# Kernel tuning notes

Measured on AMD Instinct MI355X. Metric: run time of the kernel, lower is better.

Reference implementation:

```python
import jax, jax.numpy as jnp
import numpy as np

B, N, F_IN, F_OUT = 64, 1024, 200, 200
NEG_SLOPE = 0.2  # PyG GATConv default


def setup_inputs() -> dict:
    key = jax.random.key(0)
    k1, k2, k3, k4, k5 = jax.random.split(key, 5)
    return {
        "x": jax.random.normal(k1, (B, 1, N, F_IN), dtype=jnp.float32),
        "W": jax.random.normal(k2, (F_IN, F_OUT), dtype=jnp.float32) * 0.05,
        "att_src": jax.random.normal(k3, (F_OUT,), dtype=jnp.float32) * 0.05,
        "att_dst": jax.random.normal(k4, (F_OUT,), dtype=jnp.float32) * 0.05,
        "bias": jax.random.normal(k5, (F_OUT,), dtype=jnp.float32) * 0.05,
    }


def reference(x, W, att_src, att_dst, bias):
    # x: [B, 1, N, F_IN]; module flattens to (B*N) nodes but the edge_index
    # only spans node ids 0..N-1 (complete graph minus self loops). PyG's
    # GATConv re-adds self loops for ALL B*N nodes, so:
    #   nodes 0..N-1 : dense softmax attention over all N nodes (incl. self)
    #   nodes >= N   : only the self loop -> out = h_i + bias
    b, _, n, f = x.shape
    xf = x.reshape(b * n, f)
    h = xf @ W                                # [B*N, F_OUT] linear transform

    h0 = h[:n]                                # first graph's nodes
    a_s = h0 @ att_src                        # [N] per-source score
    a_d = h0 @ att_dst                        # [N] per-target score
    # score[i, j] = leaky_relu(a_dst[i] + a_src[j]), softmax over sources j
    scores = jax.nn.leaky_relu(a_d[:, None] + a_s[None, :], negative_slope=NEG_SLOPE)
    alpha = jax.nn.softmax(scores, axis=1)    # [N, N]
    out0 = alpha @ h0 + bias                  # [N, F_OUT]

    out_rest = h[n:] + bias                   # self-loop only -> alpha == 1
    out = jnp.concatenate([out0, out_rest], axis=0)
    return out.reshape(b, n, -1)[:, None]     # [B, 1, N, F_OUT]
```

## Files before the change

### kernel.cpp

```cpp
#include <hip/hip_runtime.h>

#define BATCH 64
#define NNODE 1024
#define FDIM  200
#define MROWS (BATCH * NNODE)
#define NEG_SLOPE 0.2f

#define NKT 7
#define NNT 13
#define KTBYTES (NNT * 1024)
#define KSPLIT 4

typedef short s16x8 __attribute__((ext_vector_type(8)));
typedef float f32x4 __attribute__((ext_vector_type(4)));


__device__ __forceinline__ unsigned int f2bf(float f) {
    unsigned int u = __float_as_uint(f);
    return (u + 0x7fffu + ((u >> 16) & 1u)) >> 16;
}
__device__ __forceinline__ unsigned int pack2(float a, float b) {
    return f2bf(a) | (f2bf(b) << 16);
}

__global__ __launch_bounds__(64) void k_prep(const float* __restrict__ W,
                                             const float* __restrict__ att_src,
                                             const float* __restrict__ att_dst,
                                             unsigned short* __restrict__ fragW,
                                             float* __restrict__ wsv,
                                             float* __restrict__ wdv)
{
    const int b    = blockIdx.x;
    const int lane = threadIdx.x;

    if (b < 91) {
        const int kt   = b / NNT;
        const int nt   = b - kt * NNT;
        const int n    = nt * 16 + (lane & 15);
        const int kb   = kt * 32 + (lane >> 4) * 8;
        s16x8 v;
        #pragma unroll
        for (int j = 0; j < 8; ++j) {
            int k = kb + j;
            float f = (k < FDIM && n < FDIM) ? W[k * FDIM + n] : 0.f;
            v[j] = (short)f2bf(f);
        }
        ((s16x8*)(fragW + (size_t)b * 512))[lane] = v;
    } else {
        const int kk = b - 91;
        const float* Wr = W + kk * FDIM;
        float ps = 0.f, pd = 0.f;
        #pragma unroll
        for (int i = 0; i < 4; ++i) {
            int n = lane + i * 64;
            if (n < FDIM) {
                float wv = Wr[n];
                ps = fmaf(wv, att_src[n], ps);
                pd = fmaf(wv, att_dst[n], pd);
            }
        }
        #pragma unroll
        for (int off = 32; off; off >>= 1) {
            ps += __shfl_down(ps, off);
            pd += __shfl_down(pd, off);
        }
        if (lane == 0) { wsv[kk] = ps; wdv[kk] = pd; }
    }
}

__global__ __launch_bounds__(256) void k_av(const float* __restrict__ x,
                                            const float* __restrict__ wsv,
                                            const float* __restrict__ wdv,
                                            float* __restrict__ a_s,
                                            float* __restrict__ a_d)
{
    const int tid  = threadIdx.x;
    const int lane = tid & 63;
    const int row  = blockIdx.x * 4 + (tid >> 6);
    const float* xr = x + (size_t)row * FDIM;
    float ss = 0.f, sd = 0.f;
    for (int k = lane; k < FDIM; k += 64) {
        float xv = xr[k];
        ss = fmaf(xv, wsv[k], ss);
        sd = fmaf(xv, wdv[k], sd);
    }
    #pragma unroll
    for (int off = 32; off; off >>= 1) {
        ss += __shfl_down(ss, off);
        sd += __shfl_down(sd, off);
    }
    if (lane == 0) { a_s[row] = ss; a_d[row] = sd; }
}

__global__ __launch_bounds__(256) void k_gemm(const float* __restrict__ x,
                                              const unsigned short* __restrict__ fragW,
                                              const float* __restrict__ bias,
                                              float* __restrict__ out,
                                              unsigned short* __restrict__ h0frag)
{
    __shared__ __align__(16) unsigned short Bs[2][KTBYTES / 2];
    const int tid  = threadIdx.x;
    const int lane = tid & 63;
    const int w    = __builtin_amdgcn_readfirstlane(tid >> 6);
    const int ln   = lane & 15;
    const int quad = lane >> 4;
    const int R0   = blockIdx.x * 64;
    const int row0 = R0 + w * 16;

#define STAGE(kt_, buf_)                                                      \
    {                                                                         \
        const char* gsrc = (const char*)fragW + (size_t)(kt_) * KTBYTES;      \
        char* lbase = (char*)&Bs[buf_][0];                                    \
        _Pragma("unroll")                                                     \
        for (int i = 0; i < 4; ++i) {                                         \
            int g = i * 4 + w;                                                \
            if (g < NNT)                                                      \
                __builtin_amdgcn_global_load_lds(                             \
                    (const __attribute__((address_space(1))) void*)           \
                        (gsrc + g * 1024 + lane * 16),                        \
                    (__attribute__((address_space(3))) void*)                 \
                        (lbase + g * 1024),                                   \
                    16, 0, 0);                                                \
        }                                                                     \
    }

    f32x4 acc[NNT];
    #pragma unroll
    for (int nt = 0; nt < NNT; ++nt) acc[nt] = (f32x4){0.f, 0.f, 0.f, 0.f};

    const float* xrow = x + (size_t)(row0 + ln) * FDIM;

    float4 ar[NKT][2];
    #pragma unroll
    for (int kt = 0; kt < 4; ++kt) {
        const float4* ap = (const float4*)(xrow + kt * 32 + quad * 8);
        ar[kt][0] = ap[0]; ar[kt][1] = ap[1];
    }

    STAGE(0, 0);
    __syncthreads();

    #pragma unroll
    for (int kt = 0; kt < NKT; ++kt) {
        const int cur = kt & 1;
        if (kt < NKT - 1) STAGE(kt + 1, cur ^ 1);

        if (kt + 4 < NKT) {
            int ka = kt + 4;
            if (ka < 6) {
                const float4* ap = (const float4*)(xrow + ka * 32 + quad * 8);
                ar[ka][0] = ap[0]; ar[ka][1] = ap[1];
            } else {
                if (quad == 0) {
                    const float4* ap = (const float4*)(xrow + ka * 32);
                    ar[ka][0] = ap[0]; ar[ka][1] = ap[1];
                } else {
                    ar[ka][0] = make_float4(0.f, 0.f, 0.f, 0.f);
                    ar[ka][1] = make_float4(0.f, 0.f, 0.f, 0.f);
                }
            }
        }
        float4 f0 = ar[kt][0], f1 = ar[kt][1];
        unsigned int au[4] = {pack2(f0.x, f0.y), pack2(f0.z, f0.w),
                              pack2(f1.x, f1.y), pack2(f1.z, f1.w)};
        s16x8 a = *(s16x8*)au;

        const unsigned short* bbase = &Bs[cur][0];
        #pragma unroll
        for (int nt = 0; nt < NNT; ++nt) {
            s16x8 b = *(const s16x8*)(bbase + nt * 512 + lane * 8);
            acc[nt] = __builtin_amdgcn_mfma_f32_16x16x32_bf16(a, b, acc[nt], 0, 0, 0);
        }
        if (kt < NKT - 1) __syncthreads();
    }
#undef STAGE

    if (R0 >= NNODE) {
        #pragma unroll
        for (int nt = 0; nt < NNT; ++nt) {
            int col = nt * 16 + ln;
            if (nt < 12 || ln < 8) {
                float bv = bias[col];
                #pragma unroll
                for (int r = 0; r < 4; ++r)
                    out[(size_t)(row0 + quad * 4 + r) * FDIM + col] = acc[nt][r] + bv;
            }
        }
    } else {
        __syncthreads();
        float* scrw = (float*)&Bs[0][0] + w * (16 * 17);
        const int kt2 = row0 >> 5;
        const int lo  = (row0 >> 4) & 1;
        for (int nt = 0; nt < NNT; ++nt) {
            #pragma unroll
            for (int r = 0; r < 4; ++r) scrw[(quad * 4 + r) * 17 + ln] = acc[nt][r];
            __syncthreads();
            if (lane < 32) {
                int oct = lane >> 4, nl = lane & 15;
                uint4 dv;
                dv.x = pack2(scrw[(oct * 8 + 0) * 17 + nl], scrw[(oct * 8 + 1) * 17 + nl]);
                dv.y = pack2(scrw[(oct * 8 + 2) * 17 + nl], scrw[(oct * 8 + 3) * 17 + nl]);
                dv.z = pack2(scrw[(oct * 8 + 4) * 17 + nl], scrw[(oct * 8 + 5) * 17 + nl]);
                dv.w = pack2(scrw[(oct * 8 + 6) * 17 + nl], scrw[(oct * 8 + 7) * 17 + nl]);
                *(uint4*)(h0frag + ((size_t)(kt2 * NNT + nt) * 64 + lo * 32 + lane) * 8) = dv;
            }
            __syncthreads();
        }
    }
}

__global__ __launch_bounds__(256) void k_stats(const float* __restrict__ a_s,
                                               const float* __restrict__ a_d,
                                               const float* __restrict__ bias,
                                               float* __restrict__ out,
                                               float* __restrict__ m_out,
                                               float* __restrict__ l_out)
{
    __shared__ float as_s[1024];
    const int tid = threadIdx.x;

    if (tid < FDIM) {
        float bv = bias[tid];
        #pragma unroll
        for (int r = 0; r < 4; ++r)
            out[(size_t)(blockIdx.x * 4 + r) * FDIM + tid] = bv;
    }

    #pragma unroll
    for (int i = 0; i < 4; ++i) as_s[tid + i * 256] = a_s[tid + i * 256];
    __syncthreads();

    const int lane = tid & 63;
    const int row  = blockIdx.x * 4 + (tid >> 6);

    float mx = -1e30f;
    #pragma unroll
    for (int i = 0; i < 16; ++i) mx = fmaxf(mx, as_s[lane + i * 64]);
    #pragma unroll
    for (int off = 32; off; off >>= 1) mx = fmaxf(mx, __shfl_down(mx, off));
    mx = __shfl(mx, 0);

    const float ad = a_d[row];
    float mi = ad + mx; mi = (mi > 0.f) ? mi : NEG_SLOPE * mi;

    float sum = 0.f;
    #pragma unroll
    for (int i = 0; i < 16; ++i) {
        float s = ad + as_s[lane + i * 64];
        s = (s > 0.f) ? s : NEG_SLOPE * s;
        sum += __expf(s - mi);
    }
    #pragma unroll
    for (int off = 32; off; off >>= 1) sum += __shfl_down(sum, off);
    if (lane == 0) { m_out[row] = mi; l_out[row] = sum; }
}

__global__ __launch_bounds__(256) void k_attn(const unsigned short* __restrict__ h0frag,
                                              const float* __restrict__ a_s,
                                              const float* __restrict__ a_d,
                                              const float* __restrict__ m_v,
                                              const float* __restrict__ l_v,
                                              float* __restrict__ out)
{
    const int tid  = threadIdx.x;
    const int lane = tid & 63;
    const int w    = __builtin_amdgcn_readfirstlane(tid >> 6);
    const int ln   = lane & 15;
    const int quad = lane >> 4;
    const int bid  = blockIdx.x;
    const int kh   = bid / (16 * NNT);
    const int r2   = bid - kh * (16 * NNT);
    const int it   = r2 / NNT;
    const int nt   = r2 - it * NNT;
    const int i0   = it * 64 + w * 16;

    const float ad = a_d[i0 + ln];
    const float mi = m_v[i0 + ln];

    f32x4 accA = (f32x4){0.f, 0.f, 0.f, 0.f};
    f32x4 accB = (f32x4){0.f, 0.f, 0.f, 0.f};

    #pragma unroll
    for (int k8 = 0; k8 < 8; ++k8) {
        const int kt2 = kh * 8 + k8;
        const float4* ap = (const float4*)(a_s + kt2 * 32 + quad * 8);
        float4 f0 = ap[0], f1 = ap[1];
        float e[8] = {f0.x, f0.y, f0.z, f0.w, f1.x, f1.y, f1.z, f1.w};
        #pragma unroll
        for (int j = 0; j < 8; ++j) {
            float s = ad + e[j];
            s = (s > 0.f) ? s : NEG_SLOPE * s;
            e[j] = __expf(s - mi);
        }
        unsigned int au[4] = {pack2(e[0], e[1]), pack2(e[2], e[3]),
                              pack2(e[4], e[5]), pack2(e[6], e[7])};
        s16x8 afrag = *(s16x8*)au;
        s16x8 b = *(const s16x8*)(h0frag + ((size_t)(kt2 * NNT + nt) * 64 + lane) * 8);
        if (k8 & 1) accB = __builtin_amdgcn_mfma_f32_16x16x32_bf16(afrag, b, accB, 0, 0, 0);
        else        accA = __builtin_amdgcn_mfma_f32_16x16x32_bf16(afrag, b, accA, 0, 0, 0);
    }

    const int col = nt * 16 + ln;
    if (nt < 12 || ln < 8) {
        #pragma unroll
        for (int r = 0; r < 4; ++r) {
            float rl = 1.0f / l_v[i0 + quad * 4 + r];
            atomicAdd(&out[(size_t)(i0 + quad * 4 + r) * FDIM + col],
                      (accA[r] + accB[r]) * rl);
        }
    }
}

extern "C" void kernel_launch(void* const* d_in, const int* in_sizes, int n_in,
                              void* d_out, int out_size, void* d_ws, size_t ws_size,
                              hipStream_t stream)
{
    const float* x       = (const float*)d_in[0];
    const float* W       = (const float*)d_in[1];
    const float* att_src = (const float*)d_in[2];
    const float* att_dst = (const float*)d_in[3];
    const float* bias    = (const float*)d_in[4];
    float* out = (float*)d_out;
    char*  wsb = (char*)d_ws;

    unsigned short* h0frag = (unsigned short*)(wsb + 0);
    float* a_s   = (float*)(wsb + 425984);
    float* a_d   = (float*)(wsb + 430080);
    float* m_i   = (float*)(wsb + 434176);
    float* l_i   = (float*)(wsb + 438272);
    unsigned short* fragW = (unsigned short*)(wsb + 442368);
    float* wsv   = (float*)(wsb + 535552);
    float* wdv   = (float*)(wsb + 536352);

    k_prep <<<291,           64, 0, stream>>>(W, att_src, att_dst, fragW, wsv, wdv);
    k_av   <<<NNODE / 4,    256, 0, stream>>>(x, wsv, wdv, a_s, a_d);
    k_stats<<<NNODE / 4,    256, 0, stream>>>(a_s, a_d, bias, out, m_i, l_i);
    k_gemm <<<MROWS / 64,   256, 0, stream>>>(x, fragW, bias, out, h0frag);
    k_attn <<<KSPLIT * 16 * NNT, 256, 0, stream>>>(h0frag, a_s, a_d, m_i, l_i, out);
}
```

Baseline: 134.4 us.

## Stage two K-tiles per barrier in GEMM and reduce attention splits in LDS

The projection GEMM now loads two K-tiles of W into LDS per pipeline stage, which halves the number of barriers, and it keeps a smaller A-register prefetch window with an occupancy hint of 4 blocks. The attention kernel changes its split-K from four separate blocks that each atomically added into output to four waves in one block that sum partials through LDS. The first wave then writes the result with bias, so the bias pre-fill in k_stats and the float atomics are removed. The cost is a doubled LDS buffer in the GEMM and fewer, smaller attention blocks covering 16 rows each.

New measurement: 132.0 us. No clear change (-1.7%).

```diff
diff --git a/kernel.cpp b/kernel.cpp
--- a/kernel.cpp
+++ b/kernel.cpp
@@ -9,7 +9,6 @@
 #define NKT 7
 #define NNT 13
 #define KTBYTES (NNT * 1024)
-#define KSPLIT 4
 
 typedef short s16x8 __attribute__((ext_vector_type(8)));
 typedef float f32x4 __attribute__((ext_vector_type(4)));
@@ -92,13 +91,13 @@
     if (lane == 0) { a_s[row] = ss; a_d[row] = sd; }
 }
 
-__global__ __launch_bounds__(256) void k_gemm(const float* __restrict__ x,
-                                              const unsigned short* __restrict__ fragW,
-                                              const float* __restrict__ bias,
-                                              float* __restrict__ out,
-                                              unsigned short* __restrict__ h0frag)
-{
-    __shared__ __align__(16) unsigned short Bs[2][KTBYTES / 2];
+__global__ __launch_bounds__(256, 4) void k_gemm(const float* __restrict__ x,
+                                                 const unsigned short* __restrict__ fragW,
+                                                 const float* __restrict__ bias,
+                                                 float* __restrict__ out,
+                                                 unsigned short* __restrict__ h0frag)
+{
+    __shared__ __align__(16) unsigned short Bs[2][2 * KTBYTES / 2];
     const int tid  = threadIdx.x;
     const int lane = tid & 63;
     const int w    = __builtin_amdgcn_readfirstlane(tid >> 6);
@@ -107,14 +106,15 @@
     const int R0   = blockIdx.x * 64;
     const int row0 = R0 + w * 16;
 
-#define STAGE(kt_, buf_)                                                      \
+#define STAGE(kt0_, ntile_, buf_)                                             \
     {                                                                         \
-        const char* gsrc = (const char*)fragW + (size_t)(kt_) * KTBYTES;      \
+        const char* gsrc = (const char*)fragW + (size_t)(kt0_) * KTBYTES;     \
         char* lbase = (char*)&Bs[buf_][0];                                    \
+        const int ngroups = (ntile_) * NNT;                                   \
         _Pragma("unroll")                                                     \
-        for (int i = 0; i < 4; ++i) {                                         \
+        for (int i = 0; i < 7; ++i) {                                         \
             int g = i * 4 + w;                                                \
-            if (g < NNT)                                                      \
+            if (g < ngroups)                                                  \
                 __builtin_amdgcn_global_load_lds(                             \
                     (const __attribute__((address_space(1))) void*)           \
                         (gsrc + g * 1024 + lane * 16),                        \
@@ -124,56 +124,73 @@
         }                                                                     \
     }
 
+#define LOADA(p_, slot_)                                                      \
+    {                                                                         \
+        const int kt0_ = 2 * (p_);                                            \
+        if (kt0_ < 6) {                                                       \
+            const float4* ap = (const float4*)(xrow + kt0_ * 32 + quad * 8);  \
+            ar[slot_][0][0] = ap[0]; ar[slot_][0][1] = ap[1];                 \
+        } else {                                                              \
+            if (quad == 0) {                                                  \
+                const float4* ap = (const float4*)(xrow + kt0_ * 32);         \
+                ar[slot_][0][0] = ap[0]; ar[slot_][0][1] = ap[1];             \
+            } else {                                                          \
+                ar[slot_][0][0] = make_float4(0.f, 0.f, 0.f, 0.f);            \
+                ar[slot_][0][1] = make_float4(0.f, 0.f, 0.f, 0.f);            \
+            }                                                                 \
+        }                                                                     \
+        if (kt0_ + 1 < NKT) {                                                 \
+            const float4* ap = (const float4*)(xrow + (kt0_ + 1) * 32 + quad * 8); \
+            ar[slot_][1][0] = ap[0]; ar[slot_][1][1] = ap[1];                 \
+        }                                                                     \
+    }
+
     f32x4 acc[NNT];
     #pragma unroll
     for (int nt = 0; nt < NNT; ++nt) acc[nt] = (f32x4){0.f, 0.f, 0.f, 0.f};
 
     const float* xrow = x + (size_t)(row0 + ln) * FDIM;
-
-    float4 ar[NKT][2];
-    #pragma unroll
-    for (int kt = 0; kt < 4; ++kt) {
-        const float4* ap = (const float4*)(xrow + kt * 32 + quad * 8);
-        ar[kt][0] = ap[0]; ar[kt][1] = ap[1];
-    }
-
-    STAGE(0, 0);
+    float4 ar[2][2][2];
+
+    LOADA(0, 0);
+    STAGE(0, 2, 0);
     __syncthreads();
 
     #pragma unroll
-    for (int kt = 0; kt < NKT; ++kt) {
-        const int cur = kt & 1;
-        if (kt < NKT - 1) STAGE(kt + 1, cur ^ 1);
-
-        if (kt + 4 < NKT) {
-            int ka = kt + 4;
-            if (ka < 6) {
-                const float4* ap = (const float4*)(xrow + ka * 32 + quad * 8);
-                ar[ka][0] = ap[0]; ar[ka][1] = ap[1];
-            } else {
-                if (quad == 0) {
-                    const float4* ap = (const float4*)(xrow + ka * 32);
-                    ar[ka][0] = ap[0]; ar[ka][1] = ap[1];
-                } else {
-                    ar[ka][0] = make_float4(0.f, 0.f, 0.f, 0.f);
-                    ar[ka][1] = make_float4(0.f, 0.f, 0.f, 0.f);
-                }
-            }
-        }
-        float4 f0 = ar[kt][0], f1 = ar[kt][1];
-        unsigned int au[4] = {pack2(f0.x, f0.y), pack2(f0.z, f0.w),
-                              pack2(f1.x, f1.y), pack2(f1.z, f1.w)};
-        s16x8 a = *(s16x8*)au;
-
-        const unsigned short* bbase = &Bs[cur][0];
-        #pragma unroll
-        for (int nt = 0; nt < NNT; ++nt) {
-            s16x8 b = *(const s16x8*)(bbase + nt * 512 + lane * 8);
-            acc[nt] = __builtin_amdgcn_mfma_f32_16x16x32_bf16(a, b, acc[nt], 0, 0, 0);
-        }
-        if (kt < NKT - 1) __syncthreads();
+    for (int p = 0; p < 4; ++p) {
+        const int cur = p & 1;
+        if (p < 3) {
+            STAGE(2 * (p + 1), ((p < 2) ? 2 : 1), cur ^ 1);
+            LOADA(p + 1, cur ^ 1);
+        }
+        {
+            float4 f0 = ar[cur][0][0], f1 = ar[cur][0][1];
+            unsigned int au[4] = {pack2(f0.x, f0.y), pack2(f0.z, f0.w),
+                                  pack2(f1.x, f1.y), pack2(f1.z, f1.w)};
+            s16x8 a = *(s16x8*)au;
+            const unsigned short* bbase = &Bs[cur][0];
+            #pragma unroll
+            for (int nt = 0; nt < NNT; ++nt) {
+                s16x8 b = *(const s16x8*)(bbase + nt * 512 + lane * 8);
+                acc[nt] = __builtin_amdgcn_mfma_f32_16x16x32_bf16(a, b, acc[nt], 0, 0, 0);
+            }
+        }
+        if (p < 3) {
+            float4 f0 = ar[cur][1][0], f1 = ar[cur][1][1];
+            unsigned int au[4] = {pack2(f0.x, f0.y), pack2(f0.z, f0.w),
+                                  pack2(f1.x, f1.y), pack2(f1.z, f1.w)};
+            s16x8 a = *(s16x8*)au;
+            const unsigned short* bbase = &Bs[cur][0] + (KTBYTES / 2);
+            #pragma unroll
+            for (int nt = 0; nt < NNT; ++nt) {
+                s16x8 b = *(const s16x8*)(bbase + nt * 512 + lane * 8);
+                acc[nt] = __builtin_amdgcn_mfma_f32_16x16x32_bf16(a, b, acc[nt], 0, 0, 0);
+            }
+        }
+        __syncthreads();
     }
 #undef STAGE
+#undef LOADA
 
     if (R0 >= NNODE) {
         #pragma unroll
@@ -187,7 +204,6 @@
             }
         }
     } else {
-        __syncthreads();
         float* scrw = (float*)&Bs[0][0] + w * (16 * 17);
         const int kt2 = row0 >> 5;
         const int lo  = (row0 >> 4) & 1;
@@ -211,21 +227,11 @@
 
 __global__ __launch_bounds__(256) void k_stats(const float* __restrict__ a_s,
                                                const float* __restrict__ a_d,
-                                               const float* __restrict__ bias,
-                                               float* __restrict__ out,
                                                float* __restrict__ m_out,
                                                float* __restrict__ l_out)
 {
     __shared__ float as_s[1024];
     const int tid = threadIdx.x;
-
-    if (tid < FDIM) {
-        float bv = bias[tid];
-        #pragma unroll
-        for (int r = 0; r < 4; ++r)
-            out[(size_t)(blockIdx.x * 4 + r) * FDIM + tid] = bv;
-    }
-
     #pragma unroll
     for (int i = 0; i < 4; ++i) as_s[tid + i * 256] = a_s[tid + i * 256];
     __syncthreads();
@@ -252,7 +258,7 @@
     }
     #pragma unroll
     for (int off = 32; off; off >>= 1) sum += __shfl_down(sum, off);
-    if (lane == 0) { m_out[row] = mi; l_out[row] = sum; }
+    if (lane == 0) { m_out[row] = sum, m_out[row] = mi, l_out[row] = sum; }
 }
 
 __global__ __launch_bounds__(256) void k_attn(const unsigned short* __restrict__ h0frag,
@@ -260,19 +266,18 @@
                                               const float* __restrict__ a_d,
                                               const float* __restrict__ m_v,
                                               const float* __restrict__ l_v,
+                                              const float* __restrict__ bias,
                                               float* __restrict__ out)
 {
+    __shared__ f32x4 red[3][64];
     const int tid  = threadIdx.x;
     const int lane = tid & 63;
     const int w    = __builtin_amdgcn_readfirstlane(tid >> 6);
     const int ln   = lane & 15;
     const int quad = lane >> 4;
-    const int bid  = blockIdx.x;
-    const int kh   = bid / (16 * NNT);
-    const int r2   = bid - kh * (16 * NNT);
-    const int it   = r2 / NNT;
-    const int nt   = r2 - it * NNT;
-    const int i0   = it * 64 + w * 16;
+    const int it   = blockIdx.x / NNT;
+    const int nt   = blockIdx.x - it * NNT;
+    const int i0   = it * 16;
 
     const float ad = a_d[i0 + ln];
     const float mi = m_v[i0 + ln];
@@ -282,7 +287,7 @@
 
     #pragma unroll
     for (int k8 = 0; k8 < 8; ++k8) {
-        const int kt2 = kh * 8 + k8;
+        const int kt2 = w * 8 + k8;
         const float4* ap = (const float4*)(a_s + kt2 * 32 + quad * 8);
         float4 f0 = ap[0], f1 = ap[1];
         float e[8] = {f0.x, f0.y, f0.z, f0.w, f1.x, f1.y, f1.z, f1.w};
@@ -300,13 +305,21 @@
         else        accA = __builtin_amdgcn_mfma_f32_16x16x32_bf16(afrag, b, accA, 0, 0, 0);
     }
 
-    const int col = nt * 16 + ln;
-    if (nt < 12 || ln < 8) {
-        #pragma unroll
-        for (int r = 0; r < 4; ++r) {
-            float rl = 1.0f / l_v[i0 + quad * 4 + r];
-            atomicAdd(&out[(size_t)(i0 + quad * 4 + r) * FDIM + col],
-                      (accA[r] + accB[r]) * rl);
+    f32x4 acc = accA + accB;
+    if (w > 0) red[w - 1][lane] = acc;
+    __syncthreads();
+
+    if (w == 0) {
+        #pragma unroll
+        for (int ww = 0; ww < 3; ++ww) acc += red[ww][lane];
+        const int col = nt * 16 + ln;
+        if (nt < 12 || ln < 8) {
+            float bv = bias[col];
+            #pragma unroll
+            for (int r = 0; r < 4; ++r) {
+                float rl = 1.0f / l_v[i0 + quad * 4 + r];
+                out[(size_t)(i0 + quad * 4 + r) * FDIM + col] = acc[r] * rl + bv;
+            }
         }
     }
 }
@@ -332,9 +345,9 @@
     float* wsv   = (float*)(wsb + 535552);
     float* wdv   = (float*)(wsb + 536352);
 
-    k_prep <<<291,           64, 0, stream>>>(W, att_src, att_dst, fragW, wsv, wdv);
-    k_av   <<<NNODE / 4,    256, 0, stream>>>(x, wsv, wdv, a_s, a_d);
-    k_stats<<<NNODE / 4,    256, 0, stream>>>(a_s, a_d, bias, out, m_i, l_i);
-    k_gemm <<<MROWS / 64,   256, 0, stream>>>(x, fragW, bias, out, h0frag);
-    k_attn <<<KSPLIT * 16 * NNT, 256, 0, stream>>>(h0frag, a_s, a_d, m_i, l_i, out);
-}
+    k_prep <<<291,         64, 0, stream>>>(W, att_src, att_dst, fragW, wsv, wdv);
+    k_av   <<<NNODE / 4,  256, 0, stream>>>(x, wsv, wdv, a_s, a_d);
+    k_stats<<<NNODE / 4,  256, 0, stream>>>(a_s, a_d, m_i, l_i);
+    k_gemm <<<MROWS / 64, 256, 0, stream>>>(x, fragW, bias, out, h0frag);
+    k_attn <<<64 * NNT,   256, 0, stream>>>(h0frag, a_s, a_d, m_i, l_i, bias, out);
+}
```
